# Kernel optimization log

Measured on AMD Instinct MI355X. Metric: run time of the kernel, lower is better.

Reference implementation:

```python
import jax, jax.numpy as jnp
import numpy as np

B, C, H, W = 4, 64, 256, 256
HEADS = 8
WIN = 8            # window_size = (8, 8)
SPA_INNER = 64


def setup_inputs() -> dict:
    key = jax.random.key(0)
    ks = jax.random.split(key, 13)
    r = lambda k, s: jax.random.normal(k, s, dtype=jnp.float32)
    lin = lambda k, out_d, in_d: r(k, (out_d, in_d)) * (1.0 / np.sqrt(in_d))
    seq = WIN * WIN
    return {
        "x": r(ks[0], (B, C, H, W)),
        "pan_feature": r(ks[1], (B, C // 2, H, W)),
        "W_pan_q": lin(ks[2], SPA_INNER // 2, C // 2),
        "W_pan_k": lin(ks[3], SPA_INNER // 2, C // 2),
        "W_v1": lin(ks[4], SPA_INNER, C),
        "W_v2": lin(ks[5], SPA_INNER, C),
        "W_k2": lin(ks[6], SPA_INNER // 2, C),
        "W_q1c": lin(ks[7], SPA_INNER // 2, C),
        "W_k1c": lin(ks[8], SPA_INNER // 2, C),
        "W_inner_out": lin(ks[9], C, SPA_INNER),
        "W_inter_out": lin(ks[10], C, SPA_INNER),
        # trunc_normal_(std=1, a=-2, b=2) learned positional biases
        "pos_inner": jnp.clip(r(ks[11], (1, HEADS, seq, seq)), -2.0, 2.0),
        "pos_color": jnp.clip(r(ks[12], (1, HEADS, SPA_INNER // 2, SPA_INNER // 2)), -2.0, 2.0),
    }


def _mha(q, k, v, pos, heads, scale):
    # q,k,v: [B', n, h*d]  -> standard MHA with additive positional bias
    Bp, n, _ = q.shape
    sp = lambda t: t.reshape(Bp, n, heads, -1).transpose(0, 2, 1, 3)  # b h n d
    qh, kh, vh = sp(q) * scale, sp(k), sp(v)
    attn = jax.nn.softmax(jnp.einsum('bhid,bhjd->bhij', qh, kh) + pos, axis=-1)
    o = jnp.einsum('bhij,bhjd->bhid', attn, vh)
    return o.transpose(0, 2, 1, 3).reshape(Bp, n, -1)


def _mha_color(q, k, v, pos, heads, scale):
    # torch rearranges 'b (h d) n -> b h n d': dim1 (window area) is split
    # into heads, attention runs over the channel axis (dim2).
    Bp, hd, n = q.shape
    sp = lambda t: t.reshape(Bp, heads, hd // heads, n).transpose(0, 1, 3, 2)  # b h n d
    qh, kh, vh = sp(q) * scale, sp(k), sp(v)
    attn = jax.nn.softmax(jnp.einsum('bhid,bhjd->bhij', qh, kh) + pos, axis=-1)
    o = jnp.einsum('bhij,bhjd->bhid', attn, vh)
    return o.transpose(0, 1, 3, 2).reshape(Bp, hd, n)


def _inter_attn(q, k, v, heads):
    # elementwise cosine-similarity gating over the head-dim, no softmax
    Bp, n, dq = q.shape
    qh = q.reshape(Bp, n, heads, dq // heads).transpose(0, 2, 3, 1)  # b h d n
    kh = k.reshape(Bp, n, heads, dq // heads).transpose(0, 2, 3, 1)
    vh = v.reshape(Bp, n, heads, -1).transpose(0, 2, 1, 3)           # b h n d
    cos = jnp.sum(qh * kh, axis=2) / (jnp.linalg.norm(qh, axis=2) * jnp.linalg.norm(kh, axis=2))  # b h n
    o = cos[..., None] * vh
    return o.transpose(0, 2, 1, 3).reshape(Bp, n, -1)


def reference(x, pan_feature, W_pan_q, W_pan_k, W_v1, W_v2, W_k2, W_q1c, W_k1c,
              W_inner_out, W_inter_out, pos_inner, pos_color):
    b, c, h, w = x.shape
    hl = wl = WIN
    hn, wn = h // hl, w // wl

    def part(t):  # b c (hn hl) (wn wl) -> (b hn wn) (hl wl) c
        bb, cc = t.shape[0], t.shape[1]
        return t.reshape(bb, cc, hn, hl, wn, wl).transpose(0, 2, 4, 3, 5, 1).reshape(bb * hn * wn, hl * wl, cc)

    pan = part(pan_feature)       # [B', 64, c//2]
    xf = part(x)                  # [B', 64, c]

    pan_q = pan @ W_pan_q.T       # [B', 64, spa_inner//2]
    pan_k = pan @ W_pan_k.T
    x_v1 = xf @ W_v1.T            # [B', 64, spa_inner]
    half = x_v1.shape[-1] // 2
    v1_pan, v1_color = x_v1[..., :half], x_v1[..., half:]

    # inner spatial attention (scale uses inner_dim=spa_inner_dim, as in source)
    scale_inner = (SPA_INNER // HEADS) ** -0.5
    out_pan = _mha(pan_q, pan_k, v1_pan, pos_inner, HEADS, scale_inner)

    # inner color attention (scale uses inner_dim=window area)
    q1c = xf @ W_q1c.T
    k1c = xf @ W_k1c.T
    scale_color = ((hl * wl) // HEADS) ** -0.5
    out_color = _mha_color(q1c, k1c, v1_color, pos_color, HEADS, scale_color)

    out = jnp.concatenate([out_pan, out_color], axis=-1) @ W_inner_out.T  # [B', 64, c]
    x_v2 = out @ W_v2.T
    x_k2 = out @ W_k2.T
    out = _inter_attn(pan_q, x_k2, x_v2, HEADS)
    out = out @ W_inter_out.T     # [B', 64, c]

    cc = out.shape[-1]
    # (b hn wn) (hl wl) c -> b c (hn hl) (wn wl)
    out = out.reshape(b, hn, wn, hl, wl, cc).transpose(0, 5, 1, 3, 2, 4).reshape(b, cc, h, w)
    return out
```

## Files before the change

kernel.cpp:

```cpp
#include <hip/hip_runtime.h>


typedef __attribute__((ext_vector_type(8))) short short8;
typedef __attribute__((ext_vector_type(4))) float floatx4;

#define CCH  64
#define HH   256
#define WWD  256
#define HWsz (HH*WWD)
#define CHW  (CCH*HH*WWD)

#define PS   196
#define CV   0
#define CQ1  64
#define CK1  96
#define CPK  128
#define CPQ  160

#define OWPQ  0
#define OWPK  1024
#define OWV1  2048
#define OWV2  6144
#define OWK2  10240
#define OWQ1C 12288
#define OWK1C 14336
#define OWIO  16384
#define OWINT 20480
#define WTOT  24576

__device__ __forceinline__ unsigned int f2bf_u(float f) {
    unsigned int u = __builtin_bit_cast(unsigned int, f);
    u += 0x7FFFu + ((u >> 16) & 1u);
    return u >> 16;
}
__device__ __forceinline__ float bfu2f(unsigned int b) {
    return __builtin_bit_cast(float, b << 16);
}
__device__ __forceinline__ float rlf(float v, int l) {
    return __builtin_bit_cast(float,
        __builtin_amdgcn_readlane(__builtin_bit_cast(int, v), l));
}

union Frag { short8 v; unsigned int u[4]; };
template <int KS> struct AF { Frag ah[KS], al[KS]; };
struct HalfF { Frag h, l; };

__device__ __forceinline__ HalfF load_half(const float* __restrict__ A,
                                           int m0, int lane) {
    HalfF f;
    const int l15 = lane & 15;
    const int quad = lane >> 4;
    const float4* ap = (const float4*)(A + (m0 + l15) * PS + quad * 8);
    float4 fa = ap[0], fb = ap[1];
    float ff[8] = {fa.x, fa.y, fa.z, fa.w, fb.x, fb.y, fb.z, fb.w};
#pragma unroll
    for (int j2 = 0; j2 < 4; ++j2) {
        float f0 = ff[2 * j2], f1 = ff[2 * j2 + 1];
        unsigned int h0 = f2bf_u(f0), h1 = f2bf_u(f1);
        float r0 = f0 - bfu2f(h0), r1 = f1 - bfu2f(h1);
        f.h.u[j2] = h0 | (h1 << 16);
        f.l.u[j2] = f2bf_u(r0) | (f2bf_u(r1) << 16);
    }
    return f;
}

template <int K>
__device__ __forceinline__ AF<K / 32> load_afrag(const float* __restrict__ A,
                                                 int m0, int lane) {
    AF<K / 32> f;
#pragma unroll
    for (int kk = 0; kk < K / 32; ++kk) {
        HalfF t = load_half(A + kk * 32, m0, lane);
        f.ah[kk] = t.h; f.al[kk] = t.l;
    }
    return f;
}

template <int K, int NT>
__device__ __forceinline__ void mm(const AF<K / 32>& f,
                                   const unsigned short* __restrict__ Wh,
                                   const unsigned short* __restrict__ Wl,
                                   float* __restrict__ O,
                                   int m0, int lane) {
    const int l15 = lane & 15;
    const int quad = lane >> 4;
#pragma unroll
    for (int nt = 0; nt < NT; ++nt) {
        floatx4 acc = {0.f, 0.f, 0.f, 0.f};
#pragma unroll
        for (int kk = 0; kk < K / 32; ++kk) {
            const int wo = (nt * 16 + l15) * K + kk * 32 + quad * 8;
            short8 bh = *(const short8*)(Wh + wo);
            short8 bl = *(const short8*)(Wl + wo);
            acc = __builtin_amdgcn_mfma_f32_16x16x32_bf16(f.ah[kk].v, bh, acc, 0, 0, 0);
            acc = __builtin_amdgcn_mfma_f32_16x16x32_bf16(f.al[kk].v, bh, acc, 0, 0, 0);
            acc = __builtin_amdgcn_mfma_f32_16x16x32_bf16(f.ah[kk].v, bl, acc, 0, 0, 0);
        }
#pragma unroll
        for (int r = 0; r < 4; ++r)
            O[(m0 + quad * 4 + r) * PS + nt * 16 + l15] = acc[r];
    }
}

__global__ void cvt_w(const float* __restrict__ w0, const float* __restrict__ w1,
                      const float* __restrict__ w2, const float* __restrict__ w3,
                      const float* __restrict__ w4, const float* __restrict__ w5,
                      const float* __restrict__ w6, const float* __restrict__ w7,
                      const float* __restrict__ w8, unsigned short* __restrict__ o) {
    int i = blockIdx.x * 256 + threadIdx.x;
    const float* src; int off;
    if      (i < 1024)  { src = w0; off = 0; }
    else if (i < 2048)  { src = w1; off = 1024; }
    else if (i < 6144)  { src = w2; off = 2048; }
    else if (i < 10240) { src = w3; off = 6144; }
    else if (i < 12288) { src = w4; off = 10240; }
    else if (i < 14336) { src = w5; off = 12288; }
    else if (i < 16384) { src = w6; off = 14336; }
    else if (i < 20480) { src = w7; off = 16384; }
    else                { src = w8; off = 20480; }
    float f = src[i - off];
    unsigned int h = f2bf_u(f);
    o[i] = (unsigned short)h;
    o[WTOT + i] = (unsigned short)f2bf_u(f - bfu2f(h));
}

__global__ __launch_bounds__(256, 3) void in2ma_main(
    const float* __restrict__ x, const float* __restrict__ pan,
    const float* __restrict__ posi, const float* __restrict__ posc,
    const unsigned short* __restrict__ wb, float* __restrict__ out) {
    __shared__ __align__(16) float sp[64 * PS];

    const int tid  = threadIdx.x;
    const int wave = tid >> 6;
    const int lane = tid & 63;
    const int wid  = blockIdx.x;
    const int b    = wid >> 10;
    const int hn_i = (wid >> 5) & 31;
    const int wn_i = wid & 31;
    const int h0 = hn_i * 8, w0 = wn_i * 8;

    const float scale = 0.35355339059327373f;
    const unsigned short* wlo = wb + WTOT;
    const int s16 = wave * 16;

    {
        const int c = tid >> 2, i = tid & 3;
        const float* xp = x + (size_t)b * CHW + (size_t)c * HWsz + (size_t)h0 * WWD + w0;
#pragma unroll
        for (int r = 0; r < 2; ++r) {
            const int hl = i * 2 + r;
            const float4* p = (const float4*)(xp + hl * WWD);
            float4 a = p[0], q = p[1];
            float* d = sp + (hl * 8) * PS + CV + c;
            d[0 * PS] = a.x; d[1 * PS] = a.y; d[2 * PS] = a.z; d[3 * PS] = a.w;
            d[4 * PS] = q.x; d[5 * PS] = q.y; d[6 * PS] = q.z; d[7 * PS] = q.w;
        }
        if (tid < 128) {
            const int c2 = tid >> 2, i2 = tid & 3;
            const float* pp = pan + (size_t)b * (CHW / 2) + (size_t)c2 * HWsz
                                  + (size_t)h0 * WWD + w0;
#pragma unroll
            for (int r = 0; r < 2; ++r) {
                const int hl = i2 * 2 + r;
                const float4* p = (const float4*)(pp + hl * WWD);
                float4 a = p[0], q = p[1];
                float* d = sp + (hl * 8) * PS + CQ1 + c2;
                d[0 * PS] = a.x; d[1 * PS] = a.y; d[2 * PS] = a.z; d[3 * PS] = a.w;
                d[4 * PS] = q.x; d[5 * PS] = q.y; d[6 * PS] = q.z; d[7 * PS] = q.w;
            }
        }
    }
    __syncthreads();

    {
        AF<2> fx = load_afrag<64>(sp + CV,  s16, lane);
        AF<1> fp = load_afrag<32>(sp + CQ1, s16, lane);
        mm<64, 4>(fx, wb + OWV1,  wlo + OWV1,  sp + CV,  s16, lane);
        mm<64, 2>(fx, wb + OWQ1C, wlo + OWQ1C, sp + CQ1, s16, lane);
        mm<64, 2>(fx, wb + OWK1C, wlo + OWK1C, sp + CK1, s16, lane);
        mm<32, 2>(fp, wb + OWPQ,  wlo + OWPQ,  sp + CPQ, s16, lane);
        mm<32, 2>(fp, wb + OWPK,  wlo + OWPK,  sp + CPK, s16, lane);
    }
    __syncthreads();

#pragma unroll
    for (int hh = 0; hh < 2; ++hh) {
        const int h = wave + hh * 4;
        const float4 qv = *(const float4*)(sp + lane * PS + CPQ + 4 * h);
        const float q0 = qv.x, q1 = qv.y, q2 = qv.z, q3 = qv.w;
        const float4 kreg = *(const float4*)(sp + lane * PS + CPK + 4 * h);
        const float4 vreg = *(const float4*)(sp + lane * PS + CV  + 4 * h);
        const float4* pp4 = (const float4*)(posi + h * 4096 + lane * 64);
        float sden = 0.f;
        float o0 = 0.f, o1 = 0.f, o2 = 0.f, o3 = 0.f;
#pragma unroll
        for (int t4 = 0; t4 < 16; ++t4) {
            float4 pv = pp4[t4];
            float pvv[4] = {pv.x, pv.y, pv.z, pv.w};
#pragma unroll
            for (int u = 0; u < 4; ++u) {
                const int t = t4 * 4 + u;
                const float k0 = rlf(kreg.x, t), k1 = rlf(kreg.y, t);
                const float k2 = rlf(kreg.z, t), k3 = rlf(kreg.w, t);
                float d = q0 * k0 + q1 * k1 + q2 * k2 + q3 * k3;
                float e = __expf(d * scale + pvv[u]);
                sden += e;
                const float v0 = rlf(vreg.x, t), v1 = rlf(vreg.y, t);
                const float v2 = rlf(vreg.z, t), v3 = rlf(vreg.w, t);
                o0 += e * v0; o1 += e * v1; o2 += e * v2; o3 += e * v3;
            }
        }
        const float inv = 1.f / sden;
        float4 ov; ov.x = o0 * inv; ov.y = o1 * inv; ov.z = o2 * inv; ov.w = o3 * inv;
        *(float4*)(sp + lane * PS + CPK + 4 * h) = ov;
    }

    {
        const int h5 = wave * 2 + (lane >> 5);
        const int i5 = lane & 31;
        float q[8];
#pragma unroll
        for (int j = 0; j < 8; ++j) q[j] = sp[(8 * h5 + j) * PS + CQ1 + i5];
        float lr[32];
#pragma unroll
        for (int j = 0; j < 8; ++j) {
            const float4* kp4 = (const float4*)(sp + (8 * h5 + j) * PS + CK1);
            const float qj = q[j];
#pragma unroll
            for (int t4 = 0; t4 < 8; ++t4) {
                float4 kv = kp4[t4];
                if (j == 0) {
                    lr[4 * t4 + 0] = qj * kv.x; lr[4 * t4 + 1] = qj * kv.y;
                    lr[4 * t4 + 2] = qj * kv.z; lr[4 * t4 + 3] = qj * kv.w;
                } else {
                    lr[4 * t4 + 0] += qj * kv.x; lr[4 * t4 + 1] += qj * kv.y;
                    lr[4 * t4 + 2] += qj * kv.z; lr[4 * t4 + 3] += qj * kv.w;
                }
            }
        }
        const float4* pp4 = (const float4*)(posc + h5 * 1024 + i5 * 32);
        float sden = 0.f;
#pragma unroll
        for (int t4 = 0; t4 < 8; ++t4) {
            float4 pv = pp4[t4];
            float pvv[4] = {pv.x, pv.y, pv.z, pv.w};
#pragma unroll
            for (int u = 0; u < 4; ++u) {
                const int t = t4 * 4 + u;
                float e = __expf(lr[t] * scale + pvv[u]);
                lr[t] = e; sden += e;
            }
        }
        const float inv = 1.f / sden;
#pragma unroll
        for (int j = 0; j < 8; ++j) {
            const float4* vp4 = (const float4*)(sp + (8 * h5 + j) * PS + CV + 32);
            float acc = 0.f;
#pragma unroll
            for (int t4 = 0; t4 < 8; ++t4) {
                float4 vv = vp4[t4];
                acc += lr[4 * t4 + 0] * vv.x + lr[4 * t4 + 1] * vv.y
                     + lr[4 * t4 + 2] * vv.z + lr[4 * t4 + 3] * vv.w;
            }
            sp[(8 * h5 + j) * PS + CQ1 + i5] = acc * inv;
        }
    }
    __syncthreads();

    {
        AF<2> fc;
        { HalfF a = load_half(sp + CPK, s16, lane);
          HalfF b2 = load_half(sp + CQ1, s16, lane);
          fc.ah[0] = a.h;  fc.al[0] = a.l;
          fc.ah[1] = b2.h; fc.al[1] = b2.l; }
        mm<64, 4>(fc, wb + OWIO, wlo + OWIO, sp + CV, s16, lane);
        AF<2> fo = load_afrag<64>(sp + CV, s16, lane);
        mm<64, 4>(fo, wb + OWV2, wlo + OWV2, sp + CQ1, s16, lane);
        mm<64, 2>(fo, wb + OWK2, wlo + OWK2, sp + CPK, s16, lane);
    }
    __syncthreads();

    {
        const int t = lane;
#pragma unroll
        for (int r = 0; r < 2; ++r) {
            const int h = wave + r * 4;
            const float4 qv = *(const float4*)(sp + t * PS + CPQ + 4 * h);
            const float4 kv = *(const float4*)(sp + t * PS + CPK + 4 * h);
            float qq = qv.x * qv.x + qv.y * qv.y + qv.z * qv.z + qv.w * qv.w;
            float kk = kv.x * kv.x + kv.y * kv.y + kv.z * kv.z + kv.w * kv.w;
            float qk = qv.x * kv.x + qv.y * kv.y + qv.z * kv.z + qv.w * kv.w;
            float cosv = qk * rsqrtf(qq * kk);
            float4* vp = (float4*)(sp + t * PS + CQ1 + 8 * h);
            float4 v0 = vp[0], v1 = vp[1];
            float4 r0, r1;
            r0.x = cosv * v0.x; r0.y = cosv * v0.y; r0.z = cosv * v0.z; r0.w = cosv * v0.w;
            r1.x = cosv * v1.x; r1.y = cosv * v1.y; r1.z = cosv * v1.z; r1.w = cosv * v1.w;
            vp[0] = r0; vp[1] = r1;
        }
    }
    __syncthreads();

    {
        AF<2> f9 = load_afrag<64>(sp + CQ1, s16, lane);
        mm<64, 4>(f9, wb + OWINT, wlo + OWINT, sp + CV, s16, lane);
    }
    __syncthreads();

    {
        const int c = tid >> 2, i = tid & 3;
        float* op = out + (size_t)b * CHW + (size_t)c * HWsz + (size_t)h0 * WWD + w0;
#pragma unroll
        for (int r = 0; r < 2; ++r) {
            const int hl = i * 2 + r;
            float v[8];
#pragma unroll
            for (int wl = 0; wl < 8; ++wl)
                v[wl] = sp[(hl * 8 + wl) * PS + CV + c];
            float4 q0; q0.x = v[0]; q0.y = v[1]; q0.z = v[2]; q0.w = v[3];
            float4 q1; q1.x = v[4]; q1.y = v[5]; q1.z = v[6]; q1.w = v[7];
            float4* q = (float4*)(op + hl * WWD);
            q[0] = q0; q[1] = q1;
        }
    }
}

extern "C" void kernel_launch(void* const* d_in, const int* in_sizes, int n_in,
                              void* d_out, int out_size, void* d_ws, size_t ws_size,
                              hipStream_t stream) {
    (void)in_sizes; (void)n_in; (void)out_size; (void)ws_size;
    const float* x    = (const float*)d_in[0];
    const float* pan  = (const float*)d_in[1];
    const float* posi = (const float*)d_in[11];
    const float* posc = (const float*)d_in[12];
    unsigned short* wb = (unsigned short*)d_ws;

    cvt_w<<<WTOT / 256, 256, 0, stream>>>(
        (const float*)d_in[2], (const float*)d_in[3], (const float*)d_in[4],
        (const float*)d_in[5], (const float*)d_in[6], (const float*)d_in[7],
        (const float*)d_in[8], (const float*)d_in[9], (const float*)d_in[10], wb);

    in2ma_main<<<4096, 256, 0, stream>>>(x, pan, posi, posc, wb, (float*)d_out);
}
```

Baseline: 441.6 us.

## Double block to 512 threads and split per-window work across eight waves

Launches each window block with 8 waves instead of 4. The projection GEMMs are divided between the two wave groups, each wave takes one attention head instead of two, and the final projection is split by output-column halves. The goal is more parallelism per window and shorter serial chains per wave. In exchange it adds barriers, leaves half the waves idle in the color-attention phase, and may lower the number of resident blocks per CU because shared memory per block is unchanged.

```diff
diff --git a/kernel.cpp b/kernel.cpp
--- a/kernel.cpp
+++ b/kernel.cpp
@@ -124,7 +124,8 @@
     o[WTOT + i] = (unsigned short)f2bf_u(f - bfu2f(h));
 }
 
-__global__ __launch_bounds__(256, 3) void in2ma_main(
+__global__ __attribute__((amdgpu_flat_work_group_size(512, 512)))
+void in2ma_main(
     const float* __restrict__ x, const float* __restrict__ pan,
     const float* __restrict__ posi, const float* __restrict__ posc,
     const unsigned short* __restrict__ wb, float* __restrict__ out) {
@@ -141,33 +142,27 @@
 
     const float scale = 0.35355339059327373f;
     const unsigned short* wlo = wb + WTOT;
-    const int s16 = wave * 16;
-
-    {
-        const int c = tid >> 2, i = tid & 3;
-        const float* xp = x + (size_t)b * CHW + (size_t)c * HWsz + (size_t)h0 * WWD + w0;
-#pragma unroll
-        for (int r = 0; r < 2; ++r) {
-            const int hl = i * 2 + r;
-            const float4* p = (const float4*)(xp + hl * WWD);
-            float4 a = p[0], q = p[1];
-            float* d = sp + (hl * 8) * PS + CV + c;
-            d[0 * PS] = a.x; d[1 * PS] = a.y; d[2 * PS] = a.z; d[3 * PS] = a.w;
-            d[4 * PS] = q.x; d[5 * PS] = q.y; d[6 * PS] = q.z; d[7 * PS] = q.w;
-        }
-        if (tid < 128) {
-            const int c2 = tid >> 2, i2 = tid & 3;
+    const int s16 = (wave & 3) * 16;
+
+    {
+        const int c = lane, hl = wave;
+        const float* xp = x + (size_t)b * CHW + (size_t)c * HWsz
+                            + (size_t)(h0 + hl) * WWD + w0;
+        const float4* p = (const float4*)xp;
+        float4 a = p[0], q = p[1];
+        float* d = sp + (hl * 8) * PS + CV + c;
+        d[0 * PS] = a.x; d[1 * PS] = a.y; d[2 * PS] = a.z; d[3 * PS] = a.w;
+        d[4 * PS] = q.x; d[5 * PS] = q.y; d[6 * PS] = q.z; d[7 * PS] = q.w;
+        if (wave < 4) {
+            const int hl2 = wave * 2 + (lane >> 5);
+            const int c2 = lane & 31;
             const float* pp = pan + (size_t)b * (CHW / 2) + (size_t)c2 * HWsz
-                                  + (size_t)h0 * WWD + w0;
-#pragma unroll
-            for (int r = 0; r < 2; ++r) {
-                const int hl = i2 * 2 + r;
-                const float4* p = (const float4*)(pp + hl * WWD);
-                float4 a = p[0], q = p[1];
-                float* d = sp + (hl * 8) * PS + CQ1 + c2;
-                d[0 * PS] = a.x; d[1 * PS] = a.y; d[2 * PS] = a.z; d[3 * PS] = a.w;
-                d[4 * PS] = q.x; d[5 * PS] = q.y; d[6 * PS] = q.z; d[7 * PS] = q.w;
-            }
+                                  + (size_t)(h0 + hl2) * WWD + w0;
+            const float4* p2 = (const float4*)pp;
+            float4 a2 = p2[0], q2 = p2[1];
+            float* d2 = sp + (hl2 * 8) * PS + CQ1 + c2;
+            d2[0 * PS] = a2.x; d2[1 * PS] = a2.y; d2[2 * PS] = a2.z; d2[3 * PS] = a2.w;
+            d2[4 * PS] = q2.x; d2[5 * PS] = q2.y; d2[6 * PS] = q2.z; d2[7 * PS] = q2.w;
         }
     }
     __syncthreads();
@@ -175,17 +170,20 @@
     {
         AF<2> fx = load_afrag<64>(sp + CV,  s16, lane);
         AF<1> fp = load_afrag<32>(sp + CQ1, s16, lane);
-        mm<64, 4>(fx, wb + OWV1,  wlo + OWV1,  sp + CV,  s16, lane);
-        mm<64, 2>(fx, wb + OWQ1C, wlo + OWQ1C, sp + CQ1, s16, lane);
-        mm<64, 2>(fx, wb + OWK1C, wlo + OWK1C, sp + CK1, s16, lane);
-        mm<32, 2>(fp, wb + OWPQ,  wlo + OWPQ,  sp + CPQ, s16, lane);
-        mm<32, 2>(fp, wb + OWPK,  wlo + OWPK,  sp + CPK, s16, lane);
-    }
-    __syncthreads();
-
-#pragma unroll
-    for (int hh = 0; hh < 2; ++hh) {
-        const int h = wave + hh * 4;
+        __syncthreads();
+        if (wave < 4) {
+            mm<64, 4>(fx, wb + OWV1,  wlo + OWV1,  sp + CV,  s16, lane);
+            mm<32, 2>(fp, wb + OWPQ,  wlo + OWPQ,  sp + CPQ, s16, lane);
+        } else {
+            mm<64, 2>(fx, wb + OWQ1C, wlo + OWQ1C, sp + CQ1, s16, lane);
+            mm<64, 2>(fx, wb + OWK1C, wlo + OWK1C, sp + CK1, s16, lane);
+            mm<32, 2>(fp, wb + OWPK,  wlo + OWPK,  sp + CPK, s16, lane);
+        }
+    }
+    __syncthreads();
+
+    {
+        const int h = wave;
         const float4 qv = *(const float4*)(sp + lane * PS + CPQ + 4 * h);
         const float q0 = qv.x, q1 = qv.y, q2 = qv.z, q3 = qv.w;
         const float4 kreg = *(const float4*)(sp + lane * PS + CPK + 4 * h);
@@ -215,7 +213,7 @@
         *(float4*)(sp + lane * PS + CPK + 4 * h) = ov;
     }
 
-    {
+    if (wave < 4) {
         const int h5 = wave * 2 + (lane >> 5);
         const int i5 = lane & 31;
         float q[8];
@@ -273,55 +271,54 @@
           HalfF b2 = load_half(sp + CQ1, s16, lane);
           fc.ah[0] = a.h;  fc.al[0] = a.l;
           fc.ah[1] = b2.h; fc.al[1] = b2.l; }
+        __syncthreads();
         mm<64, 4>(fc, wb + OWIO, wlo + OWIO, sp + CV, s16, lane);
         AF<2> fo = load_afrag<64>(sp + CV, s16, lane);
-        mm<64, 4>(fo, wb + OWV2, wlo + OWV2, sp + CQ1, s16, lane);
-        mm<64, 2>(fo, wb + OWK2, wlo + OWK2, sp + CPK, s16, lane);
-    }
-    __syncthreads();
-
-    {
-        const int t = lane;
-#pragma unroll
-        for (int r = 0; r < 2; ++r) {
-            const int h = wave + r * 4;
-            const float4 qv = *(const float4*)(sp + t * PS + CPQ + 4 * h);
-            const float4 kv = *(const float4*)(sp + t * PS + CPK + 4 * h);
-            float qq = qv.x * qv.x + qv.y * qv.y + qv.z * qv.z + qv.w * qv.w;
-            float kk = kv.x * kv.x + kv.y * kv.y + kv.z * kv.z + kv.w * kv.w;
-            float qk = qv.x * kv.x + qv.y * kv.y + qv.z * kv.z + qv.w * kv.w;
-            float cosv = qk * rsqrtf(qq * kk);
-            float4* vp = (float4*)(sp + t * PS + CQ1 + 8 * h);
-            float4 v0 = vp[0], v1 = vp[1];
-            float4 r0, r1;
-            r0.x = cosv * v0.x; r0.y = cosv * v0.y; r0.z = cosv * v0.z; r0.w = cosv * v0.w;
-            r1.x = cosv * v1.x; r1.y = cosv * v1.y; r1.z = cosv * v1.z; r1.w = cosv * v1.w;
-            vp[0] = r0; vp[1] = r1;
-        }
-    }
-    __syncthreads();
-
-    {
-        AF<2> f9 = load_afrag<64>(sp + CQ1, s16, lane);
-        mm<64, 4>(f9, wb + OWINT, wlo + OWINT, sp + CV, s16, lane);
-    }
-    __syncthreads();
-
-    {
-        const int c = tid >> 2, i = tid & 3;
-        float* op = out + (size_t)b * CHW + (size_t)c * HWsz + (size_t)h0 * WWD + w0;
-#pragma unroll
-        for (int r = 0; r < 2; ++r) {
-            const int hl = i * 2 + r;
-            float v[8];
-#pragma unroll
-            for (int wl = 0; wl < 8; ++wl)
-                v[wl] = sp[(hl * 8 + wl) * PS + CV + c];
-            float4 q0; q0.x = v[0]; q0.y = v[1]; q0.z = v[2]; q0.w = v[3];
-            float4 q1; q1.x = v[4]; q1.y = v[5]; q1.z = v[6]; q1.w = v[7];
-            float4* q = (float4*)(op + hl * WWD);
-            q[0] = q0; q[1] = q1;
-        }
+        if (wave < 4)
+            mm<64, 4>(fo, wb + OWV2, wlo + OWV2, sp + CQ1, s16, lane);
+        else
+            mm<64, 2>(fo, wb + OWK2, wlo + OWK2, sp + CPK, s16, lane);
+    }
+    __syncthreads();
+
+    {
+        const int t = lane, h = wave;
+        const float4 qv = *(const float4*)(sp + t * PS + CPQ + 4 * h);
+        const float4 kv = *(const float4*)(sp + t * PS + CPK + 4 * h);
+        float qq = qv.x * qv.x + qv.y * qv.y + qv.z * qv.z + qv.w * qv.w;
+        float kk = kv.x * kv.x + kv.y * kv.y + kv.z * kv.z + kv.w * kv.w;
+        float qk = qv.x * kv.x + qv.y * kv.y + qv.z * kv.z + qv.w * kv.w;
+        float cosv = qk * rsqrtf(qq * kk);
+        float4* vp = (float4*)(sp + t * PS + CQ1 + 8 * h);
+        float4 v0 = vp[0], v1 = vp[1];
+        float4 r0, r1;
+        r0.x = cosv * v0.x; r0.y = cosv * v0.y; r0.z = cosv * v0.z; r0.w = cosv * v0.w;
+        r1.x = cosv * v1.x; r1.y = cosv * v1.y; r1.z = cosv * v1.z; r1.w = cosv * v1.w;
+        vp[0] = r0; vp[1] = r1;
+    }
+    __syncthreads();
+
+    {
+        const int st = (wave >> 1) * 16;
+        const int half = wave & 1;
+        AF<2> f9 = load_afrag<64>(sp + CQ1, st, lane);
+        mm<64, 2>(f9, wb + OWINT + half * 32 * 64, wlo + OWINT + half * 32 * 64,
+                  sp + CV + half * 32, st, lane);
+    }
+    __syncthreads();
+
+    {
+        const int c = lane, hl = wave;
+        float* op = out + (size_t)b * CHW + (size_t)c * HWsz
+                        + (size_t)(h0 + hl) * WWD + w0;
+        float v[8];
+#pragma unroll
+        for (int wl = 0; wl < 8; ++wl)
+            v[wl] = sp[(hl * 8 + wl) * PS + CV + c];
+        float4 q0; q0.x = v[0]; q0.y = v[1]; q0.z = v[2]; q0.w = v[3];
+        float4 q1; q1.x = v[4]; q1.y = v[5]; q1.z = v[6]; q1.w = v[7];
+        float4* q = (float4*)op;
+        q[0] = q0; q[1] = q1;
     }
 }
 
@@ -340,5 +337,5 @@
         (const float*)d_in[5], (const float*)d_in[6], (const float*)d_in[7],
         (const float*)d_in[8], (const float*)d_in[9], (const float*)d_in[10], wb);
 
-    in2ma_main<<<4096, 256, 0, stream>>>(x, pan, posi, posc, wb, (float*)d_out);
-}
+    in2ma_main<<<4096, 512, 0, stream>>>(x, pan, posi, posc, wb, (float*)d_out);
+}
```

New measurement: 545.9 us. 23.6% more time.
